# Performance work log

Hardware: AMD Instinct MI355X
Metric: run time of the kernel (lower is better)

Reference implementation:

```python
import jax, jax.numpy as jnp
import numpy as np

# Model hyperparameters (match init_kwargs)
D_MODEL = 1024
D_STATE = 16
D_CONV = 4
EXPAND = 2
NUM_BLOCKS = 4
D_INNER = EXPAND * D_MODEL            # 2048
DT_RANK = (D_MODEL + 15) // 16        # 64 (math.ceil(d_model/16), Mamba default)
BATCH, SEQLEN = 2, 1024


def setup_inputs() -> dict:
    key = jax.random.key(0)
    ks = jax.random.split(key, 16)
    s = 0.02  # init scale for random weights
    inp = {
        "x": jax.random.normal(ks[0], (BATCH, SEQLEN), jnp.float32),
        # embedding: nn.Linear(1, d_model)
        "emb_w": jax.random.normal(ks[1], (D_MODEL, 1), jnp.float32) * s,
        "emb_b": jax.random.normal(ks[2], (D_MODEL,), jnp.float32) * s,
        # per-block Mamba params, stacked on leading num_blocks axis
        "in_proj_w": jax.random.normal(ks[3], (NUM_BLOCKS, 2 * D_INNER, D_MODEL), jnp.float32) * s,
        "conv_w": jax.random.normal(ks[4], (NUM_BLOCKS, D_INNER, D_CONV), jnp.float32) * s,
        "conv_b": jax.random.normal(ks[5], (NUM_BLOCKS, D_INNER), jnp.float32) * s,
        "x_proj_w": jax.random.normal(ks[6], (NUM_BLOCKS, DT_RANK + 2 * D_STATE, D_INNER), jnp.float32) * s,
        "dt_proj_w": jax.random.normal(ks[7], (NUM_BLOCKS, D_INNER, DT_RANK), jnp.float32) * s,
        "dt_proj_b": jax.random.normal(ks[8], (NUM_BLOCKS, D_INNER), jnp.float32) * s,
        # A = -exp(A_log); standard S4D-real init: A_log = log(1..d_state)
        "A_log": jnp.broadcast_to(
            jnp.log(jnp.arange(1, D_STATE + 1, dtype=jnp.float32)),
            (NUM_BLOCKS, D_INNER, D_STATE)).copy(),
        "D_param": jnp.ones((NUM_BLOCKS, D_INNER), jnp.float32),
        "out_proj_w": jax.random.normal(ks[9], (NUM_BLOCKS, D_MODEL, D_INNER), jnp.float32) * s,
    }
    return inp


def _mamba_block(h, in_w, cw, cb, xp_w, dt_w, dt_b, A_log, Dp, out_w):
    B, L, _ = h.shape
    xz = jnp.einsum("bld,ed->ble", h, in_w)          # [B,L,2*Di]
    xx, z = jnp.split(xz, 2, axis=-1)                  # each [B,L,Di]

    # causal depthwise conv1d (padding=d_conv-1, truncated to L)
    xpad = jnp.pad(xx, ((0, 0), (D_CONV - 1, 0), (0, 0)))
    xc = cb
    for k in range(D_CONV):
        xc = xc + cw[:, k] * jax.lax.dynamic_slice_in_dim(xpad, k, L, axis=1)
    u = jax.nn.silu(xc)                                 # [B,L,Di]

    x_dbl = jnp.einsum("bld,ed->ble", u, xp_w)        # [B,L,dt_rank+2N]
    dt_lo = x_dbl[..., :DT_RANK]
    Bm = x_dbl[..., DT_RANK:DT_RANK + D_STATE]         # [B,L,N]
    Cm = x_dbl[..., DT_RANK + D_STATE:]                # [B,L,N]
    dt = jax.nn.softplus(jnp.einsum("blr,dr->bld", dt_lo, dt_w) + dt_b)  # [B,L,Di]

    A = -jnp.exp(A_log)                                 # [Di,N]

    def step(hst, ins):
        dt_t, B_t, C_t, u_t = ins                       # [B,Di],[B,N],[B,N],[B,Di]
        dA = jnp.exp(dt_t[:, :, None] * A)              # [B,Di,N]
        hst = dA * hst + (dt_t * u_t)[:, :, None] * B_t[:, None, :]
        y_t = jnp.einsum("bdn,bn->bd", hst, C_t)
        return hst, y_t

    xs = (dt.transpose(1, 0, 2), Bm.transpose(1, 0, 2),
          Cm.transpose(1, 0, 2), u.transpose(1, 0, 2))
    h0 = jnp.zeros((B, D_INNER, D_STATE), h.dtype)
    _, ys = jax.lax.scan(step, h0, xs)                  # [L,B,Di]
    y = ys.transpose(1, 0, 2) + Dp * u                  # skip term D*u
    y = y * jax.nn.silu(z)                              # gated
    return jnp.einsum("bld,ed->ble", y, out_w)        # [B,L,D]


def reference(x, emb_w, emb_b, in_proj_w, conv_w, conv_b, x_proj_w,
              dt_proj_w, dt_proj_b, A_log, D_param, out_proj_w):
    # embedding: Linear(1 -> d_model) on x.unsqueeze(-1)
    h = x[..., None] * emb_w[:, 0] + emb_b              # [B,L,D]
    for i in range(NUM_BLOCKS):
        h = _mamba_block(h, in_proj_w[i], conv_w[i], conv_b[i], x_proj_w[i],
                         dt_proj_w[i], dt_proj_b[i], A_log[i], D_param[i],
                         out_proj_w[i])
        h = jax.nn.silu(h)                               # activation after each block
    return h
```

## Files before the change

kernel.cpp:

```cpp
#include <hip/hip_runtime.h>
#include <math.h>

#define D_MODEL  1024
#define D_STATE  16
#define D_CONV   4
#define D_INNER  2048
#define DT_RANK  64
#define NUM_BLK  4
#define BATCH    2
#define SEQLEN   1024
#define ML       (BATCH*SEQLEN)
#define XPROJ_N  (DT_RANK + 2*D_STATE)
#define XPROJ_NP 128
#define CH       32
#define CL       32
#define XKSPL    16

typedef __attribute__((ext_vector_type(8))) short short8;
typedef __attribute__((ext_vector_type(4))) float f32x4;

__device__ __forceinline__ float silu_f(float x) {
    return x / (1.0f + __expf(-x));
}
__device__ __forceinline__ float softplus_f(float x) {
    if (x > 15.0f) return x;
    return __logf(1.0f + __expf(x));
}
__device__ __forceinline__ unsigned short f2bf(float x) {
    unsigned int u = __float_as_uint(x);
    u += 0x7FFFu + ((u >> 16) & 1u);
    return (unsigned short)(u >> 16);
}
__device__ __forceinline__ float bf2f(unsigned short h) {
    return __uint_as_float(((unsigned int)h) << 16);
}

__global__ __launch_bounds__(256) void embed_kernel(
    const float* __restrict__ x, const float* __restrict__ ew,
    const float* __restrict__ eb,
    unsigned short* __restrict__ h_hi, unsigned short* __restrict__ h_lo)
{
    int t  = blockIdx.x * 256 + threadIdx.x;
    int d  = t & (D_MODEL - 1);
    int bl = t >> 10;
    float v = fmaf(x[bl], ew[d], eb[d]);
    unsigned short h16 = f2bf(v);
    h_hi[t] = h16;
    h_lo[t] = f2bf(v - bf2f(h16));
}

__global__ __launch_bounds__(256) void tobf16_kernel(
    const float* __restrict__ src, unsigned short* __restrict__ dst, int n4)
{
    int t = blockIdx.x * 256 + threadIdx.x;
    if (t >= n4) return;
    float4 v = ((const float4*)src)[t];
    ushort4 h;
    h.x = f2bf(v.x); h.y = f2bf(v.y); h.z = f2bf(v.z); h.w = f2bf(v.w);
    ((ushort4*)dst)[t] = h;
}

__global__ __launch_bounds__(256) void xpw_pad_kernel(
    const float* __restrict__ src, unsigned short* __restrict__ dst)
{
    int t  = blockIdx.x * 256 + threadIdx.x;
    int k4 = t & 511;
    int n  = (t >> 9) & 127;
    int i  = t >> 16;
    ushort4 h = {0, 0, 0, 0};
    if (n < XPROJ_N) {
        float4 v = *(const float4*)(src + ((size_t)(i * XPROJ_N + n) * D_INNER + k4 * 4));
        h.x = f2bf(v.x); h.y = f2bf(v.y); h.z = f2bf(v.z); h.w = f2bf(v.w);
    }
    *(ushort4*)(dst + ((size_t)(i * XPROJ_NP + n) * D_INNER + k4 * 4)) = h;
}

__global__ __launch_bounds__(256) void conv_split_kernel(
    const float* __restrict__ xz, const float* __restrict__ cw,
    const float* __restrict__ cb,
    unsigned short* __restrict__ u_hi, unsigned short* __restrict__ u_lo)
{
    int t  = blockIdx.x * 256 + threadIdx.x;
    int d4 = t & (D_INNER / 4 - 1);
    int bl = t >> 9;
    int l  = bl & (SEQLEN - 1);
    int d  = d4 * 4;

    const float* base = xz + (size_t)bl * (2 * D_INNER) + d;
    float4 z4 = make_float4(0.f, 0.f, 0.f, 0.f);
    float4 x3 = *(const float4*)base;
    float4 x2 = (l >= 1) ? *(const float4*)(base - 1 * (2 * D_INNER)) : z4;
    float4 x1 = (l >= 2) ? *(const float4*)(base - 2 * (2 * D_INNER)) : z4;
    float4 x0 = (l >= 3) ? *(const float4*)(base - 3 * (2 * D_INNER)) : z4;
    float4 c0 = *(const float4*)(cw + (d + 0) * 4);
    float4 c1 = *(const float4*)(cw + (d + 1) * 4);
    float4 c2 = *(const float4*)(cw + (d + 2) * 4);
    float4 c3 = *(const float4*)(cw + (d + 3) * 4);
    float4 cbv = *(const float4*)(cb + d);

    float u0 = silu_f(cbv.x + c0.x*x0.x + c0.y*x1.x + c0.z*x2.x + c0.w*x3.x);
    float u1 = silu_f(cbv.y + c1.x*x0.y + c1.y*x1.y + c1.z*x2.y + c1.w*x3.y);
    float u2 = silu_f(cbv.z + c2.x*x0.z + c2.y*x1.z + c2.z*x2.z + c2.w*x3.z);
    float u3 = silu_f(cbv.w + c3.x*x0.w + c3.y*x1.w + c3.z*x2.w + c3.w*x3.w);

    ushort4 h, lo;
    h.x = f2bf(u0); lo.x = f2bf(u0 - bf2f(h.x));
    h.y = f2bf(u1); lo.y = f2bf(u1 - bf2f(h.y));
    h.z = f2bf(u2); lo.z = f2bf(u2 - bf2f(h.z));
    h.w = f2bf(u3); lo.w = f2bf(u3 - bf2f(h.w));
    ((ushort4*)u_hi)[t] = h;
    ((ushort4*)u_lo)[t] = lo;
}

template<int BM, int BN, int WM, int WN, int EPI, int KSPLIT>
__global__ __launch_bounds__(WM*WN*64) void mfma_gemm(
    const unsigned short* __restrict__ Ahi, const unsigned short* __restrict__ Alo,
    const unsigned short* __restrict__ Whi,
    float* __restrict__ Cf, unsigned short* __restrict__ Chi,
    unsigned short* __restrict__ Clo, const float* __restrict__ bias,
    int M, int N, int K)
{
    constexpr int NW  = WM * WN;
    constexpr int WTM = BM / WM;
    constexpr int WTN = BN / WN;
    constexpr int MT  = WTM / 16;
    constexpr int NT  = WTN / 16;
    constexpr int NCH = (2*BM + BN) / 16;
    constexpr int CPW = NCH / NW;

    __shared__ unsigned short lds[(2*BM + BN) * 32];

    const int tid  = threadIdx.x;
    const int wave = tid >> 6;
    const int lane = tid & 63;
    const int m0 = blockIdx.y * BM;
    const int n0 = blockIdx.x * BN;
    const int wm0 = (wave % WM) * WTM;
    const int wn0 = (wave / WM) * WTN;
    const int lrow = lane & 15;
    const int kqi  = lane >> 4;

    const int rc = lane >> 2;
    const int po = ((lane & 3) - (rc >> 1)) & 3;

    const unsigned short* gsrc[CPW];
    unsigned short* ldst[CPW];
    #pragma unroll
    for (int cc = 0; cc < CPW; cc++) {
        int c  = wave * CPW + cc;
        int r0 = c * 16;
        const unsigned short* s; int row;
        if      (r0 < BM)        { s = Ahi; row = m0 + r0; }
        else if (r0 < 2*BM)      { s = Alo; row = m0 + r0 - BM; }
        else                     { s = Whi; row = n0 + r0 - 2*BM; }
        gsrc[cc] = s + (size_t)(row + rc) * K + po * 8;
        ldst[cc] = &lds[c * 512];
    }

    f32x4 acc[MT][NT] = {};

    const int kseg = K / KSPLIT;
    const int kz   = (KSPLIT > 1) ? blockIdx.z : 0;
    const int kbeg = kz * kseg;
    const int kend = kbeg + kseg;

    for (int kt = kbeg; kt < kend; kt += 32) {
        __syncthreads();
        #pragma unroll
        for (int cc = 0; cc < CPW; cc++)
            __builtin_amdgcn_global_load_lds(
                (const __attribute__((address_space(1))) unsigned int*)(gsrc[cc] + kt),
                (__attribute__((address_space(3))) unsigned int*)ldst[cc],
                16, 0, 0);
        asm volatile("s_waitcnt vmcnt(0)" ::: "memory");
        __syncthreads();

        short8 ahi[MT], alo[MT], bhi[NT];
        #pragma unroll
        for (int i = 0; i < MT; i++) {
            int r = wm0 + i * 16 + lrow;
            int o = (kqi + ((r >> 1) & 3)) & 3;
            ahi[i] = *(const short8*)&lds[r * 32 + o * 8];
            alo[i] = *(const short8*)&lds[(BM + r) * 32 + o * 8];
        }
        #pragma unroll
        for (int j = 0; j < NT; j++) {
            int r = wn0 + j * 16 + lrow;
            int o = (kqi + ((r >> 1) & 3)) & 3;
            bhi[j] = *(const short8*)&lds[(2*BM + r) * 32 + o * 8];
        }
        #pragma unroll
        for (int i = 0; i < MT; i++)
            #pragma unroll
            for (int j = 0; j < NT; j++) {
                acc[i][j] = __builtin_amdgcn_mfma_f32_16x16x32_bf16(ahi[i], bhi[j], acc[i][j], 0, 0, 0);
                acc[i][j] = __builtin_amdgcn_mfma_f32_16x16x32_bf16(alo[i], bhi[j], acc[i][j], 0, 0, 0);
            }
    }

    const int orow = (lane >> 4) * 4;
    float* Cfz = Cf + (KSPLIT > 1 ? (size_t)kz * M * N : 0);
    #pragma unroll
    for (int i = 0; i < MT; i++) {
        #pragma unroll
        for (int j = 0; j < NT; j++) {
            #pragma unroll
            for (int r = 0; r < 4; r++) {
                int gm = m0 + wm0 + i * 16 + orow + r;
                int gn = n0 + wn0 + j * 16 + lrow;
                size_t off = (size_t)gm * N + gn;
                float v = acc[i][j][r];
                if (KSPLIT > 1 || EPI == 0) {
                    Cfz[off] = v;
                } else if (EPI == 1) {
                    Cf[off] = silu_f(v);
                } else if (EPI == 3) {
                    Cf[off] = softplus_f(v + bias[gn]);
                } else {
                    float s = silu_f(v);
                    unsigned short h16 = f2bf(s);
                    Chi[off] = h16;
                    Clo[off] = f2bf(s - bf2f(h16));
                }
            }
        }
    }
}

template<int FINAL>
__global__ __launch_bounds__(256) void oproj_reduce(
    const float* __restrict__ P, float* __restrict__ outf,
    unsigned short* __restrict__ hi, unsigned short* __restrict__ lo)
{
    int t = blockIdx.x * 256 + threadIdx.x;
    float4 a = ((const float4*)P)[t];
    float4 b = ((const float4*)(P + (size_t)ML * D_MODEL))[t];
    float4 s;
    s.x = silu_f(a.x + b.x); s.y = silu_f(a.y + b.y);
    s.z = silu_f(a.z + b.z); s.w = silu_f(a.w + b.w);
    if (FINAL) {
        ((float4*)outf)[t] = s;
    } else {
        ushort4 h, l;
        h.x = f2bf(s.x); l.x = f2bf(s.x - bf2f(h.x));
        h.y = f2bf(s.y); l.y = f2bf(s.y - bf2f(h.y));
        h.z = f2bf(s.z); l.z = f2bf(s.z - bf2f(h.z));
        h.w = f2bf(s.w); l.w = f2bf(s.w - bf2f(h.w));
        ((ushort4*)hi)[t] = h;
        ((ushort4*)lo)[t] = l;
    }
}

__global__ __launch_bounds__(256) void xproj_reduce2(
    const float* __restrict__ P, float* __restrict__ xd,
    unsigned short* __restrict__ dh, unsigned short* __restrict__ dl)
{
    int t = blockIdx.x * 256 + threadIdx.x;
    int m = t >> 5;
    int c = (t & 31) * 4;
    if (c >= XPROJ_N) return;
    const float* p = P + (size_t)m * XPROJ_NP + c;
    float4 s = *(const float4*)p;
    #pragma unroll
    for (int z = 1; z < XKSPL; z++) {
        float4 v = *(const float4*)(p + (size_t)z * ML * XPROJ_NP);
        s.x += v.x; s.y += v.y; s.z += v.z; s.w += v.w;
    }
    *(float4*)(xd + (size_t)m * XPROJ_N + c) = s;
    if (c < DT_RANK) {
        ushort4 h, l;
        h.x = f2bf(s.x); l.x = f2bf(s.x - bf2f(h.x));
        h.y = f2bf(s.y); l.y = f2bf(s.y - bf2f(h.y));
        h.z = f2bf(s.z); l.z = f2bf(s.z - bf2f(h.z));
        h.w = f2bf(s.w); l.w = f2bf(s.w - bf2f(h.w));
        *(ushort4*)(dh + (size_t)m * DT_RANK + c) = h;
        *(ushort4*)(dl + (size_t)m * DT_RANK + c) = l;
    }
}

__global__ __launch_bounds__(256) void scan_pass1(
    const float* __restrict__ dt,
    const unsigned short* __restrict__ u_hi, const unsigned short* __restrict__ u_lo,
    const float* __restrict__ xdbl, const float* __restrict__ A_log,
    float* __restrict__ s_arr, float* __restrict__ sdt_arr)
{
    int d = blockIdx.x * 256 + threadIdx.x;
    int j = blockIdx.y;
    int b = blockIdx.z;

    float Av[D_STATE];
    #pragma unroll
    for (int n = 0; n < D_STATE; n++)
        Av[n] = -__expf(A_log[d * D_STATE + n]);

    float st[D_STATE] = {};
    float sdt = 0.f;

    size_t idx = ((size_t)(b * SEQLEN + j * CL)) * D_INNER + d;
    const float* xr = xdbl + (size_t)(b * SEQLEN + j * CL) * XPROJ_N + DT_RANK;

    for (int l = 0; l < CL; l++) {
        float uv  = bf2f(u_hi[idx]) + bf2f(u_lo[idx]);
        float dtv = dt[idx];
        float du  = dtv * uv;
        sdt += dtv;
        float4 B0 = *(const float4*)(xr + 0);
        float4 B1 = *(const float4*)(xr + 4);
        float4 B2 = *(const float4*)(xr + 8);
        float4 B3 = *(const float4*)(xr + 12);
        float Bv[16] = {B0.x,B0.y,B0.z,B0.w, B1.x,B1.y,B1.z,B1.w,
                        B2.x,B2.y,B2.z,B2.w, B3.x,B3.y,B3.z,B3.w};
        #pragma unroll
        for (int n = 0; n < D_STATE; n++)
            st[n] = fmaf(st[n], __expf(dtv * Av[n]), du * Bv[n]);
        idx += D_INNER;
        xr  += XPROJ_N;
    }

    size_t base = (size_t)(b * CH + j) * D_STATE * D_INNER + d;
    #pragma unroll
    for (int n = 0; n < D_STATE; n++)
        s_arr[base + (size_t)n * D_INNER] = st[n];
    sdt_arr[(size_t)(b * CH + j) * D_INNER + d] = sdt;
}

__global__ __launch_bounds__(256) void scan_pass2(
    const float* __restrict__ A_log, const float* __restrict__ sdt_arr,
    float* __restrict__ s_arr)
{
    int t = blockIdx.x * 256 + threadIdx.x;
    int d = t & (D_INNER - 1);
    int n = (t >> 11) & (D_STATE - 1);
    int b = t >> 15;

    float Av = -__expf(A_log[d * D_STATE + n]);
    float init = 0.f;
    for (int j = 0; j < CH; j++) {
        size_t off = ((size_t)(b * CH + j) * D_STATE + n) * D_INNER + d;
        float sv  = s_arr[off];
        float sdt = sdt_arr[(size_t)(b * CH + j) * D_INNER + d];
        s_arr[off] = init;
        init = fmaf(init, __expf(Av * sdt), sv);
    }
}

__global__ __launch_bounds__(256) void scan_pass3(
    const float* __restrict__ dt,
    const unsigned short* __restrict__ u_hi, const unsigned short* __restrict__ u_lo,
    const float* __restrict__ xz, const float* __restrict__ xdbl,
    const float* __restrict__ A_log, const float* __restrict__ Dp,
    const float* __restrict__ s_arr,
    unsigned short* __restrict__ y_hi, unsigned short* __restrict__ y_lo)
{
    int d = blockIdx.x * 256 + threadIdx.x;
    int j = blockIdx.y;
    int b = blockIdx.z;

    float Av[D_STATE];
    #pragma unroll
    for (int n = 0; n < D_STATE; n++)
        Av[n] = -__expf(A_log[d * D_STATE + n]);
    float Dd = Dp[d];

    float st[D_STATE];
    size_t sbase = (size_t)(b * CH + j) * D_STATE * D_INNER + d;
    #pragma unroll
    for (int n = 0; n < D_STATE; n++)
        st[n] = s_arr[sbase + (size_t)n * D_INNER];

    size_t idx  = ((size_t)(b * SEQLEN + j * CL)) * D_INNER + d;
    size_t zidx = ((size_t)(b * SEQLEN + j * CL)) * (2 * D_INNER) + D_INNER + d;
    const float* xr = xdbl + (size_t)(b * SEQLEN + j * CL) * XPROJ_N + DT_RANK;

    for (int l = 0; l < CL; l++) {
        float uv  = bf2f(u_hi[idx]) + bf2f(u_lo[idx]);
        float dtv = dt[idx];
        float du  = dtv * uv;
        float4 B0 = *(const float4*)(xr + 0);
        float4 B1 = *(const float4*)(xr + 4);
        float4 B2 = *(const float4*)(xr + 8);
        float4 B3 = *(const float4*)(xr + 12);
        float4 C0 = *(const float4*)(xr + 16);
        float4 C1 = *(const float4*)(xr + 20);
        float4 C2 = *(const float4*)(xr + 24);
        float4 C3 = *(const float4*)(xr + 28);
        float Bv[16] = {B0.x,B0.y,B0.z,B0.w, B1.x,B1.y,B1.z,B1.w,
                        B2.x,B2.y,B2.z,B2.w, B3.x,B3.y,B3.z,B3.w};
        float Cv[16] = {C0.x,C0.y,C0.z,C0.w, C1.x,C1.y,C1.z,C1.w,
                        C2.x,C2.y,C2.z,C2.w, C3.x,C3.y,C3.z,C3.w};
        float yt = 0.f;
        #pragma unroll
        for (int n = 0; n < D_STATE; n++) {
            float s = fmaf(st[n], __expf(dtv * Av[n]), du * Bv[n]);
            st[n] = s;
            yt = fmaf(s, Cv[n], yt);
        }
        float zv = xz[zidx];
        float yv = (yt + Dd * uv) * silu_f(zv);
        unsigned short h16 = f2bf(yv);
        y_hi[idx] = h16;
        y_lo[idx] = f2bf(yv - bf2f(h16));

        idx  += D_INNER;
        zidx += 2 * D_INNER;
        xr   += XPROJ_N;
    }
}

extern "C" void kernel_launch(void* const* d_in, const int* in_sizes, int n_in,
                              void* d_out, int out_size, void* d_ws, size_t ws_size,
                              hipStream_t stream)
{
    const float* x     = (const float*)d_in[0];
    const float* emb_w = (const float*)d_in[1];
    const float* emb_b = (const float*)d_in[2];
    const float* inw   = (const float*)d_in[3];
    const float* cw    = (const float*)d_in[4];
    const float* cb    = (const float*)d_in[5];
    const float* xpw   = (const float*)d_in[6];
    const float* dtw   = (const float*)d_in[7];
    const float* dtb   = (const float*)d_in[8];
    const float* Alog  = (const float*)d_in[9];
    const float* Dpar  = (const float*)d_in[10];
    const float* outw  = (const float*)d_in[11];

    float* out = (float*)d_out;

    float* ws    = (float*)d_ws;
    float* xz    = ws;
    float* xd    = xz + 8388608;
    float* dtbuf = xd + 196608;
    float* sdt   = dtbuf + 4194304;
    float* s_arr = sdt + 131072;
    unsigned short* u_hi = (unsigned short*)(s_arr + 2097152);
    unsigned short* u_lo = u_hi + 4194304;
    unsigned short* h_hi = u_hi;
    unsigned short* h_lo = u_lo;
    unsigned short* y_hi = u_lo + 4194304;
    unsigned short* y_lo = y_hi + 4194304;
    unsigned short* dtlo_hi = y_lo + 4194304;
    unsigned short* dtlo_lo = dtlo_hi + 131072;
    unsigned short* wih_all = dtlo_lo + 131072;
    unsigned short* woh_all = wih_all + 4 * 4194304;
    unsigned short* wxp_all = woh_all + 4 * 2097152;
    unsigned short* wdt_all = wxp_all + 4 * 262144;

    tobf16_kernel<<<(NUM_BLK * 1048576 + 255) / 256, 256, 0, stream>>>(
        inw, wih_all, NUM_BLK * 1048576);
    tobf16_kernel<<<(NUM_BLK * 524288 + 255) / 256, 256, 0, stream>>>(
        outw, woh_all, NUM_BLK * 524288);
    tobf16_kernel<<<(NUM_BLK * 32768 + 255) / 256, 256, 0, stream>>>(
        dtw, wdt_all, NUM_BLK * 32768);
    xpw_pad_kernel<<<(NUM_BLK * XPROJ_NP * 512) / 256, 256, 0, stream>>>(
        xpw, wxp_all);

    embed_kernel<<<(ML * D_MODEL) / 256, 256, 0, stream>>>(x, emb_w, emb_b, h_hi, h_lo);

    for (int i = 0; i < NUM_BLK; i++) {
        const float* cw_i   = cw   + (size_t)i * D_INNER * D_CONV;
        const float* cb_i   = cb   + (size_t)i * D_INNER;
        const float* dtb_i  = dtb  + (size_t)i * D_INNER;
        const float* Alog_i = Alog + (size_t)i * D_INNER * D_STATE;
        const float* Dp_i   = Dpar + (size_t)i * D_INNER;
        unsigned short* wih = wih_all + (size_t)i * 4194304;
        unsigned short* woh = woh_all + (size_t)i * 2097152;
        unsigned short* wxp = wxp_all + (size_t)i * 262144;
        unsigned short* wdt = wdt_all + (size_t)i * 131072;

        mfma_gemm<128, 128, 2, 4, 0, 1><<<dim3(32, 16), 512, 0, stream>>>(
            h_hi, h_lo, wih, xz, nullptr, nullptr, nullptr, ML, 2 * D_INNER, D_MODEL);

        conv_split_kernel<<<(ML * D_INNER / 4) / 256, 256, 0, stream>>>(
            xz, cw_i, cb_i, u_hi, u_lo);

        mfma_gemm<64, 128, 2, 4, 0, XKSPL><<<dim3(1, 32, XKSPL), 512, 0, stream>>>(
            u_hi, u_lo, wxp, dtbuf, nullptr, nullptr, nullptr, ML, XPROJ_NP, D_INNER);

        xproj_reduce2<<<(ML * 32) / 256, 256, 0, stream>>>(
            dtbuf, xd, dtlo_hi, dtlo_lo);

        mfma_gemm<64, 128, 2, 4, 3, 1><<<dim3(16, 32), 512, 0, stream>>>(
            dtlo_hi, dtlo_lo, wdt, dtbuf, nullptr, nullptr, dtb_i,
            ML, D_INNER, DT_RANK);

        scan_pass1<<<dim3(D_INNER / 256, CH, BATCH), 256, 0, stream>>>(
            dtbuf, u_hi, u_lo, xd, Alog_i, s_arr, sdt);
        scan_pass2<<<(BATCH * D_INNER * D_STATE) / 256, 256, 0, stream>>>(
            Alog_i, sdt, s_arr);
        scan_pass3<<<dim3(D_INNER / 256, CH, BATCH), 256, 0, stream>>>(
            dtbuf, u_hi, u_lo, xz, xd, Alog_i, Dp_i, s_arr, y_hi, y_lo);

        mfma_gemm<64, 128, 2, 4, 0, 2><<<dim3(8, 32, 2), 512, 0, stream>>>(
            y_hi, y_lo, woh, xz, nullptr, nullptr, nullptr, ML, D_MODEL, D_INNER);

        if (i == NUM_BLK - 1) {
            oproj_reduce<1><<<(ML * D_MODEL / 4) / 256, 256, 0, stream>>>(
                xz, out, nullptr, nullptr);
        } else {
            oproj_reduce<0><<<(ML * D_MODEL / 4) / 256, 256, 0, stream>>>(
                xz, nullptr, h_hi, h_lo);
        }
    }
}
```

Before: 806.3 us.

## Double-buffer GEMM LDS loads and fold scan pass2 into pass3

The MFMA GEMM now double-buffers its LDS tiles, issuing the next K-step's global-to-LDS loads before computing on the current buffer and waiting with a partial vmcnt. This hides global load latency behind MFMA work, at the cost of twice the LDS per block, which may lower occupancy. Separately, the serial inter-chunk prefix pass (scan_pass2) is removed. Each pass3 block now recomputes its own initial state by walking all earlier chunk summaries, which saves a launch but adds redundant work that grows with chunk index.

```diff
diff --git a/kernel.cpp b/kernel.cpp
--- a/kernel.cpp
+++ b/kernel.cpp
@@ -127,8 +127,11 @@
     constexpr int NT  = WTN / 16;
     constexpr int NCH = (2*BM + BN) / 16;
     constexpr int CPW = NCH / NW;
-
-    __shared__ unsigned short lds[(2*BM + BN) * 32];
+    constexpr int LDSU = (2*BM + BN) * 32;
+    static_assert(CPW * NW == NCH, "chunk split must be exact");
+    static_assert(CPW >= 2 && CPW <= 4, "vmcnt literal table");
+
+    __shared__ unsigned short lds[2 * LDSU];
 
     const int tid  = threadIdx.x;
     const int wave = tid >> 6;
@@ -164,30 +167,46 @@
     const int kbeg = kz * kseg;
     const int kend = kbeg + kseg;
 
+    #pragma unroll
+    for (int cc = 0; cc < CPW; cc++)
+        __builtin_amdgcn_global_load_lds(
+            (const __attribute__((address_space(1))) unsigned int*)(gsrc[cc] + kbeg),
+            (__attribute__((address_space(3))) unsigned int*)ldst[cc],
+            16, 0, 0);
+
+    int cur = 0;
     for (int kt = kbeg; kt < kend; kt += 32) {
-        __syncthreads();
-        #pragma unroll
-        for (int cc = 0; cc < CPW; cc++)
-            __builtin_amdgcn_global_load_lds(
-                (const __attribute__((address_space(1))) unsigned int*)(gsrc[cc] + kt),
-                (__attribute__((address_space(3))) unsigned int*)ldst[cc],
-                16, 0, 0);
-        asm volatile("s_waitcnt vmcnt(0)" ::: "memory");
-        __syncthreads();
+        if (kt + 32 < kend) {
+            #pragma unroll
+            for (int cc = 0; cc < CPW; cc++)
+                __builtin_amdgcn_global_load_lds(
+                    (const __attribute__((address_space(1))) unsigned int*)(gsrc[cc] + kt + 32),
+                    (__attribute__((address_space(3))) unsigned int*)(ldst[cc] + (cur ^ 1) * LDSU),
+                    16, 0, 0);
+            if constexpr (CPW == 2)      asm volatile("s_waitcnt vmcnt(2)" ::: "memory");
+            else if constexpr (CPW == 3) asm volatile("s_waitcnt vmcnt(3)" ::: "memory");
+            else                         asm volatile("s_waitcnt vmcnt(4)" ::: "memory");
+        } else {
+            asm volatile("s_waitcnt vmcnt(0)" ::: "memory");
+        }
+        __builtin_amdgcn_s_barrier();
+        __builtin_amdgcn_sched_barrier(0);
+
+        const unsigned short* L = lds + cur * LDSU;
 
         short8 ahi[MT], alo[MT], bhi[NT];
         #pragma unroll
         for (int i = 0; i < MT; i++) {
             int r = wm0 + i * 16 + lrow;
             int o = (kqi + ((r >> 1) & 3)) & 3;
-            ahi[i] = *(const short8*)&lds[r * 32 + o * 8];
-            alo[i] = *(const short8*)&lds[(BM + r) * 32 + o * 8];
+            ahi[i] = *(const short8*)&L[r * 32 + o * 8];
+            alo[i] = *(const short8*)&L[(BM + r) * 32 + o * 8];
         }
         #pragma unroll
         for (int j = 0; j < NT; j++) {
             int r = wn0 + j * 16 + lrow;
             int o = (kqi + ((r >> 1) & 3)) & 3;
-            bhi[j] = *(const short8*)&lds[(2*BM + r) * 32 + o * 8];
+            bhi[j] = *(const short8*)&L[(2*BM + r) * 32 + o * 8];
         }
         #pragma unroll
         for (int i = 0; i < MT; i++)
@@ -196,6 +215,9 @@
                 acc[i][j] = __builtin_amdgcn_mfma_f32_16x16x32_bf16(ahi[i], bhi[j], acc[i][j], 0, 0, 0);
                 acc[i][j] = __builtin_amdgcn_mfma_f32_16x16x32_bf16(alo[i], bhi[j], acc[i][j], 0, 0, 0);
             }
+        __builtin_amdgcn_sched_barrier(0);
+        __builtin_amdgcn_s_barrier();
+        cur ^= 1;
     }
 
     const int orow = (lane >> 4) * 4;
@@ -324,32 +346,12 @@
     sdt_arr[(size_t)(b * CH + j) * D_INNER + d] = sdt;
 }
 
-__global__ __launch_bounds__(256) void scan_pass2(
-    const float* __restrict__ A_log, const float* __restrict__ sdt_arr,
-    float* __restrict__ s_arr)
-{
-    int t = blockIdx.x * 256 + threadIdx.x;
-    int d = t & (D_INNER - 1);
-    int n = (t >> 11) & (D_STATE - 1);
-    int b = t >> 15;
-
-    float Av = -__expf(A_log[d * D_STATE + n]);
-    float init = 0.f;
-    for (int j = 0; j < CH; j++) {
-        size_t off = ((size_t)(b * CH + j) * D_STATE + n) * D_INNER + d;
-        float sv  = s_arr[off];
-        float sdt = sdt_arr[(size_t)(b * CH + j) * D_INNER + d];
-        s_arr[off] = init;
-        init = fmaf(init, __expf(Av * sdt), sv);
-    }
-}
-
-__global__ __launch_bounds__(256) void scan_pass3(
+__global__ __launch_bounds__(256) void scan_pass23(
     const float* __restrict__ dt,
     const unsigned short* __restrict__ u_hi, const unsigned short* __restrict__ u_lo,
     const float* __restrict__ xz, const float* __restrict__ xdbl,
     const float* __restrict__ A_log, const float* __restrict__ Dp,
-    const float* __restrict__ s_arr,
+    const float* __restrict__ s_arr, const float* __restrict__ sdt_arr,
     unsigned short* __restrict__ y_hi, unsigned short* __restrict__ y_lo)
 {
     int d = blockIdx.x * 256 + threadIdx.x;
@@ -362,11 +364,14 @@
         Av[n] = -__expf(A_log[d * D_STATE + n]);
     float Dd = Dp[d];
 
-    float st[D_STATE];
-    size_t sbase = (size_t)(b * CH + j) * D_STATE * D_INNER + d;
-    #pragma unroll
-    for (int n = 0; n < D_STATE; n++)
-        st[n] = s_arr[sbase + (size_t)n * D_INNER];
+    float st[D_STATE] = {};
+    for (int i = 0; i < j; i++) {
+        float sdtv = sdt_arr[(size_t)(b * CH + i) * D_INNER + d];
+        size_t sb  = (size_t)(b * CH + i) * D_STATE * D_INNER + d;
+        #pragma unroll
+        for (int n = 0; n < D_STATE; n++)
+            st[n] = fmaf(st[n], __expf(Av[n] * sdtv), s_arr[sb + (size_t)n * D_INNER]);
+    }
 
     size_t idx  = ((size_t)(b * SEQLEN + j * CL)) * D_INNER + d;
     size_t zidx = ((size_t)(b * SEQLEN + j * CL)) * (2 * D_INNER) + D_INNER + d;
@@ -485,10 +490,8 @@
 
         scan_pass1<<<dim3(D_INNER / 256, CH, BATCH), 256, 0, stream>>>(
             dtbuf, u_hi, u_lo, xd, Alog_i, s_arr, sdt);
-        scan_pass2<<<(BATCH * D_INNER * D_STATE) / 256, 256, 0, stream>>>(
-            Alog_i, sdt, s_arr);
-        scan_pass3<<<dim3(D_INNER / 256, CH, BATCH), 256, 0, stream>>>(
-            dtbuf, u_hi, u_lo, xz, xd, Alog_i, Dp_i, s_arr, y_hi, y_lo);
+        scan_pass23<<<dim3(D_INNER / 256, CH, BATCH), 256, 0, stream>>>(
+            dtbuf, u_hi, u_lo, xz, xd, Alog_i, Dp_i, s_arr, sdt, y_hi, y_lo);
 
         mfma_gemm<64, 128, 2, 4, 0, 2><<<dim3(8, 32, 2), 512, 0, stream>>>(
             y_hi, y_lo, woh, xz, nullptr, nullptr, nullptr, ML, D_MODEL, D_INNER);
```

Measured after the change: 879.3 us. +9.1%, slower.
